# Kernel optimization log

Measured on AMD Instinct MI355X. Metric: run time of the kernel, lower is better.

## Reference

```python
import jax, jax.numpy as jnp
import numpy as np

NH = 8          # attention heads
TEMP = 2.0      # gumbel temperature


def _gumbel_softmax_hard(logits, key, temperature):
    # hard=True straight-through gumbel softmax (module is in eval mode)
    g = jax.random.gumbel(key, logits.shape, logits.dtype)
    y = jax.nn.softmax((logits + g) / temperature, axis=-1)
    y_hard = jax.nn.one_hot(jnp.argmax(y, axis=-1), logits.shape[-1], dtype=y.dtype)
    return y_hard - jax.lax.stop_gradient(y) + y


def _experts(x, w1, w2, w3):
    # SwiGLU FFN over all experts at once: x [T,C], w1/w3 [E,H,C], w2 [E,C,H] -> [T,E,C]
    h = jax.nn.silu(jnp.einsum('tc,ehc->teh', x, w1)) * jnp.einsum('tc,ehc->teh', x, w3)
    return jnp.einsum('teh,ech->tec', h, w2)


def _mha(q_in, kv_in, in_w, in_b, out_w, out_b):
    C = q_in.shape[-1]
    hd = C // NH
    q = q_in @ in_w[:C].T + in_b[:C]
    k = kv_in @ in_w[C:2 * C].T + in_b[C:2 * C]
    v = kv_in @ in_w[2 * C:].T + in_b[2 * C:]
    B, Tq, _ = q.shape
    Tk = k.shape[1]
    q = q.reshape(B, Tq, NH, hd)
    k = k.reshape(B, Tk, NH, hd)
    v = v.reshape(B, Tk, NH, hd)
    scale = jnp.asarray(1.0 / np.sqrt(hd), q.dtype)
    att = jax.nn.softmax(jnp.einsum('bqhd,bkhd->bhqk', q, k) * scale, axis=-1)
    o = jnp.einsum('bhqk,bkhd->bqhd', att, v).reshape(B, Tq, C)
    return o @ out_w.T + out_b


def setup_inputs() -> dict:
    key = jax.random.key(0)
    ks = jax.random.split(key, 20)
    B, T, S, C, E, H = 2, 2048, 77, 1024, 4, 2816
    p = lambda k, sh: jax.random.normal(k, sh, jnp.float32) * 0.02
    return {
        'x': jax.random.normal(ks[0], (B, T, C), jnp.float32),
        'time': jax.random.normal(ks[1], (B,), jnp.float32),
        'caption': jax.random.normal(ks[2], (B, S, C), jnp.float32),
        'language': jax.random.randint(ks[3], (B,), 0, 9),
        'lang_embed': p(ks[4], (9, C)),
        'lang_gate_w': p(ks[5], (E, C)),
        'lang_gate_b': jnp.zeros((E,), jnp.float32),
        'lang_w1': p(ks[6], (E, H, C)),
        'lang_w2': p(ks[7], (E, C, H)),
        'lang_w3': p(ks[8], (E, H, C)),
        'in_proj_w': p(ks[9], (3 * C, C)),
        'in_proj_b': jnp.zeros((3 * C,), jnp.float32),
        'out_proj_w': p(ks[10], (C, C)),
        'out_proj_b': jnp.zeros((C,), jnp.float32),
        'cap_gate_w': p(ks[11], (E, C)),
        'cap_gate_b': jnp.zeros((E,), jnp.float32),
        'cap_w1': p(ks[12], (E, H, C)),
        'cap_w2': p(ks[13], (E, C, H)),
        'cap_w3': p(ks[14], (E, H, C)),
    }


def reference(x, time, caption, language, lang_embed, lang_gate_w, lang_gate_b,
              lang_w1, lang_w2, lang_w3, in_proj_w, in_proj_b, out_proj_w, out_proj_b,
              cap_gate_w, cap_gate_b, cap_w1, cap_w2, cap_w3):
    B, T, C = x.shape
    x_flat = x.reshape(-1, C)                                   # [B*T, C]

    # language gating (one logit vector per batch element, repeated over T tokens)
    lang_emb = lang_embed[language]                             # [B, C]
    lang_logits = lang_emb @ lang_gate_w.T + lang_gate_b        # [B, E]
    lang_probs = _gumbel_softmax_hard(lang_logits, jax.random.key(1), TEMP)
    lang_probs = jnp.repeat(lang_probs, T, axis=0)              # [B*T, E]

    lang_outputs = _experts(x_flat, lang_w1, lang_w2, lang_w3)  # [B*T, E, C]
    first_out = (lang_outputs * lang_probs[:, :, None]).sum(axis=1)  # [B*T, C]
    first_reshaped = first_out.reshape(B, T, C)

    # cross attention against caption, then per-token caption gating
    cross = _mha(first_reshaped, caption, in_proj_w, in_proj_b, out_proj_w, out_proj_b)
    cross_flat = cross.reshape(-1, C)
    cap_logits = cross_flat @ cap_gate_w.T + cap_gate_b         # [B*T, E]
    cap_probs = _gumbel_softmax_hard(cap_logits, jax.random.key(2), TEMP)

    cap_outputs = _experts(first_out, cap_w1, cap_w2, cap_w3)   # [B*T, E, C]
    second_out = (cap_outputs * cap_probs[:, :, None]).sum(axis=1)

    total_out = (first_out + second_out).reshape(B, T, C)

    all_probs = jnp.concatenate([lang_probs, cap_probs], axis=1)  # [B*T, 2E]
    expert_usage = all_probs.mean(axis=0)
    loss = (expert_usage * jnp.log(expert_usage + 1e-10)).sum()
    return total_out, loss
```

## Files before the change

### kernel.cpp

```cpp
#include <hip/hip_runtime.h>
#include <stdint.h>

#define B_ 2
#define T_ 2048
#define S_ 77
#define C_ 1024
#define E_ 4
#define H_ 2816
#define NH_ 8
#define HD_ 128
#define N_ (B_*T_)
#define MAXGB (N_/128 + E_)
#define MAXGB2 (N_/256 + E_)
#define PEsz ((size_t)H_*C_)

typedef _Float16 h8 __attribute__((ext_vector_type(8)));
typedef _Float16 h4 __attribute__((ext_vector_type(4)));
typedef float f4 __attribute__((ext_vector_type(4)));

__device__ __forceinline__ void gload16(const void* g, void* l){
  __builtin_amdgcn_global_load_lds((const __attribute__((address_space(1))) void*)g,
                                   (__attribute__((address_space(3))) void*)l, 16, 0, 0);
}

__device__ __forceinline__ void xcd_swizzle(int& bx, int& by){
  int nx = gridDim.x, ny = gridDim.y;
  int nwg = nx*ny;
  int wg = by*nx + bx;
  int q = nwg >> 3, r = nwg & 7;
  int xcd = wg & 7, idx = wg >> 3;
  int s = (xcd < r ? xcd*(q+1) : r*(q+1) + (xcd-r)*q) + idx;
  bx = s % nx; by = s / nx;
}

__device__ __forceinline__ uint32_t rotl32(uint32_t v, int r){ return (v<<r)|(v>>(32-r)); }
__device__ __forceinline__ void threefry2x32(uint32_t k0, uint32_t k1,
                                             uint32_t x, uint32_t y,
                                             uint32_t& o0, uint32_t& o1){
  uint32_t k2 = k0 ^ k1 ^ 0x1BD11BDAu;
  x += k0; y += k1;
#define TFR(r) { x += y; y = rotl32(y, r); y ^= x; }
  TFR(13) TFR(15) TFR(26) TFR(6)   x += k1; y += k2 + 1u;
  TFR(17) TFR(29) TFR(16) TFR(24)  x += k2; y += k0 + 2u;
  TFR(13) TFR(15) TFR(26) TFR(6)   x += k0; y += k1 + 3u;
  TFR(17) TFR(29) TFR(16) TFR(24)  x += k1; y += k2 + 4u;
  TFR(13) TFR(15) TFR(26) TFR(6)   x += k2; y += k0 + 5u;
#undef TFR
  o0 = x; o1 = y;
}
__device__ __forceinline__ float gumbel_from_bits(uint32_t bits){
  const float TINY = 1.17549435e-38f;
  float f = __uint_as_float((bits >> 9) | 0x3f800000u) - 1.0f;
  float u = fmaxf(TINY, f + TINY);
  return -logf(-logf(u));
}
__device__ __forceinline__ float jax_gumbel(uint32_t k0, uint32_t k1, uint32_t idx){
  uint32_t a, b;
  threefry2x32(k0, k1, 0u, idx, a, b);
  return gumbel_from_bits(a ^ b);
}

__global__ __launch_bounds__(256) void setup_lang(
    const float* __restrict__ lang_embed, const float* __restrict__ gate_w,
    const float* __restrict__ gate_b, const int* __restrict__ language,
    float* __restrict__ langP, int* __restrict__ lang_sel, int* __restrict__ counts)
{
  __shared__ float red[256];
  __shared__ float logits[8];
  int tid = threadIdx.x;
  for (int be = 0; be < 8; ++be){
    int b = be >> 2, e = be & 3;
    const float* emb = lang_embed + (size_t)language[b] * C_;
    const float* gw  = gate_w + (size_t)e * C_;
    float p = 0.f;
    for (int c = tid; c < C_; c += 256) p += emb[c] * gw[c];
    red[tid] = p; __syncthreads();
    for (int s = 128; s > 0; s >>= 1){
      if (tid < s) red[tid] += red[tid + s];
      __syncthreads();
    }
    if (tid == 0) logits[be] = red[0] + gate_b[e];
    __syncthreads();
  }
  if (tid == 0){
    for (int b = 0; b < B_; ++b){
      float z[E_], m = -3.4e38f;
      for (int e = 0; e < E_; ++e){
        float gmb = jax_gumbel(0u, 1u, (uint32_t)(b*E_ + e));
        z[e] = (logits[b*E_ + e] + gmb) * 0.5f;
        m = fmaxf(m, z[e]);
      }
      float y[E_], sum = 0.f;
      for (int e = 0; e < E_; ++e){ y[e] = expf(z[e] - m); sum += y[e]; }
      for (int e = 0; e < E_; ++e) y[e] = y[e] / sum;
      int best = 0; float bv = y[0];
      for (int e = 1; e < E_; ++e) if (y[e] > bv){ bv = y[e]; best = e; }
      lang_sel[b] = best;
      for (int e = 0; e < E_; ++e)
        langP[b*E_ + e] = ((e == best) ? 1.0f : 0.0f) - y[e] + y[e];
    }
    for (int e = 0; e < E_; ++e) counts[e] = 0;
  }
}

__global__ __launch_bounds__(256) void conv_split(const float* __restrict__ s,
    _Float16* __restrict__ hi, _Float16* __restrict__ lo, long n4){
  long i = (long)blockIdx.x*256 + threadIdx.x;
  long stride = (long)gridDim.x*256;
  for (; i < n4; i += stride){
    float4 v = ((const float4*)s)[i];
    h4 h, L;
    h[0]=(_Float16)v.x; h[1]=(_Float16)v.y; h[2]=(_Float16)v.z; h[3]=(_Float16)v.w;
    L[0]=(_Float16)(v.x-(float)h[0]); L[1]=(_Float16)(v.y-(float)h[1]);
    L[2]=(_Float16)(v.z-(float)h[2]); L[3]=(_Float16)(v.w-(float)h[3]);
    ((h4*)hi)[i] = h; ((h4*)lo)[i] = L;
  }
}
__global__ __launch_bounds__(256) void conv_plain(const float* __restrict__ s,
    _Float16* __restrict__ d, long n4){
  long i = (long)blockIdx.x*256 + threadIdx.x;
  long stride = (long)gridDim.x*256;
  for (; i < n4; i += stride){
    float4 v = ((const float4*)s)[i];
    h4 h;
    h[0]=(_Float16)v.x; h[1]=(_Float16)v.y; h[2]=(_Float16)v.z; h[3]=(_Float16)v.w;
    ((h4*)d)[i] = h;
  }
}
__global__ __launch_bounds__(256) void conv_split_sel(const float* __restrict__ base,
    const int* __restrict__ sel, int slot,
    _Float16* __restrict__ hi, _Float16* __restrict__ lo, long n4){
  const float* s = base + (size_t)sel[slot]*PEsz;
  long i = (long)blockIdx.x*256 + threadIdx.x;
  long stride = (long)gridDim.x*256;
  for (; i < n4; i += stride){
    float4 v = ((const float4*)s)[i];
    h4 h, L;
    h[0]=(_Float16)v.x; h[1]=(_Float16)v.y; h[2]=(_Float16)v.z; h[3]=(_Float16)v.w;
    L[0]=(_Float16)(v.x-(float)h[0]); L[1]=(_Float16)(v.y-(float)h[1]);
    L[2]=(_Float16)(v.z-(float)h[2]); L[3]=(_Float16)(v.w-(float)h[3]);
    ((h4*)hi)[i] = h; ((h4*)lo)[i] = L;
  }
}
template<bool SPLIT>
__global__ __launch_bounds__(256) void conv_w13(
    const float* __restrict__ w1, const float* __restrict__ w3,
    const int* __restrict__ sel, int nslot,
    _Float16* __restrict__ hi, _Float16* __restrict__ lo)
{
  const int K8 = C_/8;
  long total = (long)nslot * (2*H_) * K8;
  for (long i = (long)blockIdx.x*256 + threadIdx.x; i < total; i += (long)gridDim.x*256){
    int kv = (int)(i & (K8-1));
    long rs = i >> 7;
    int r  = (int)(rs % (2*H_));
    int slot = (int)(rs / (2*H_));
    int e = SPLIT ? sel[slot] : slot;
    int gg = r >> 5, o = r & 31;
    const float* src = ((o<16)? w1 : w3) + (size_t)e*PEsz + (size_t)(16*gg + (o&15))*C_ + kv*8;
    float4 v0 = *(const float4*)src, v1 = *(const float4*)(src+4);
    float vv[8] = {v0.x,v0.y,v0.z,v0.w,v1.x,v1.y,v1.z,v1.w};
    h8 hh, ll;
#pragma unroll
    for (int jj=0;jj<8;++jj){
      hh[jj] = (_Float16)vv[jj];
      if constexpr (SPLIT) ll[jj] = (_Float16)(vv[jj]-(float)hh[jj]);
    }
    size_t dof = (size_t)slot*2*PEsz + (size_t)r*C_ + kv*8;
    *(h8*)(hi + dof) = hh;
    if constexpr (SPLIT) *(h8*)(lo + dof) = ll;
  }
}

__global__ __launch_bounds__(512,2) void gemm_gate_split(
    const _Float16* __restrict__ Ahi, const _Float16* __restrict__ Alo,
    const _Float16* __restrict__ Bhi, const _Float16* __restrict__ Blo,
    _Float16* __restrict__ Hhi, _Float16* __restrict__ Hlo)
{
  __shared__ __align__(16) char smem[147456];
  const int tid = threadIdx.x, w = tid>>6, l = tid&63;
  const int lm = l&15, g = l>>4;
  const int wm = w>>1, wn = w&1;
  int bx = blockIdx.x, by = blockIdx.y;
  xcd_swizzle(bx, by);
  const int n0 = bx<<7;
  const int m0 = by<<8;
  const size_t eoff = (m0 >= T_) ? (size_t)2*PEsz : 0;

  const _Float16* srcA[4]; const _Float16* srcB[2];
#pragma unroll
  for (int jj=0;jj<4;++jj){
    int c = jj*512 + tid, r = c>>3, s = c&7;
    int st = s ^ (r&7);
    srcA[jj] = (st<4 ? Ahi : Alo) + (size_t)(m0 + r)*C_ + ((st&3)<<3);
  }
#pragma unroll
  for (int jj=0;jj<2;++jj){
    int c = jj*512 + tid, r = c>>3, s = c&7;
    int st = s ^ (r&7);
    srcB[jj] = (st<4 ? Bhi : Blo) + eoff + (size_t)(n0 + r)*C_ + ((st&3)<<3);
  }

#define STG(ts, bi) { \
    int k0 = (ts)<<5; \
    char* db = smem + (bi)*49152; \
    _Pragma("unroll") \
    for (int jj=0;jj<4;++jj) gload16(srcA[jj]+k0, db + (jj*512 + w*64)*16); \
    _Pragma("unroll") \
    for (int jj=0;jj<2;++jj) gload16(srcB[jj]+k0, db + 32768 + (jj*512 + w*64)*16); \
  }

  const int shi = (g ^ (lm&7)) << 4;
  int aoff[4], boff[4];
#pragma unroll
  for (int i=0;i<4;++i){
    aoff[i] = ((wm*64 + i*16 + lm)<<7) + shi;
    boff[i] = 32768 + ((wn*64 + i*16 + lm)<<7) + shi;
  }

  f4 acc[4][4] = {};
  const int nt = C_/32;
  STG(0,0) STG(1,1)
  for (int t=0; t<nt; ++t){
    const int bi = t%3;
// ... 104 lines not shown
#pragma unroll
  for (int i=0;i<4;++i){
    aoff[i] = ((wm*64 + i*16 + lm)<<7) + shi;
    boff[i] = 32768 + ((wn*64 + i*16 + lm)<<7) + shi;
  }

  f4 acc[4][4] = {};
  const int nt = C_/64;
  STG(0,0) STG(1,1)
  for (int t=0; t<nt; ++t){
    const int bi = t%3;
    const int ts = (t+2 < nt) ? t+2 : 0;
    STG(ts, (t+2)%3)
    asm volatile("s_waitcnt vmcnt(12)" ::: "memory");
    __builtin_amdgcn_s_barrier();
    asm volatile("" ::: "memory");
    const char* base = smem + bi*49152;
#pragma unroll
    for (int kk=0;kk<2;++kk){
      h8 af[4], bf[4];
      const int x = kk<<6;
#pragma unroll
      for (int i=0;i<4;++i){ af[i] = *(const h8*)(base + (aoff[i]^x)); bf[i] = *(const h8*)(base + (boff[i]^x)); }
      __builtin_amdgcn_s_setprio(1);
#pragma unroll
      for (int mi=0;mi<4;++mi)
#pragma unroll
        for (int ni=0;ni<4;++ni)
          acc[mi][ni] = __builtin_amdgcn_mfma_f32_16x16x32_f16(af[mi], bf[ni], acc[mi][ni],0,0,0);
      __builtin_amdgcn_s_setprio(0);
    }
    asm volatile("" ::: "memory");
    __builtin_amdgcn_s_barrier();
  }
#undef STG

#pragma unroll
  for (int mi=0;mi<4;++mi){
#pragma unroll
    for (int p=0;p<2;++p){
      int hc = ((n0 + wn*64)>>1) + p*16 + lm;
#pragma unroll
      for (int j=0;j<4;++j){
        int rl = wm*64 + mi*16 + (g<<2) + j;
        if (rl >= valid) continue;
        float s1 = acc[mi][2*p][j], s3 = acc[mi][2*p+1][j];
        Hout[(size_t)(m0 + rl)*H_ + hc] = (_Float16)(s1/(1.f+expf(-s1))*s3);
      }
    }
  }
}

template<int EPI, int NSEG, int EXPM>
__global__ __launch_bounds__(256,2) void gemm8(
    const _Float16* __restrict__ A0, const _Float16* __restrict__ A1,
    const _Float16* __restrict__ B0, const _Float16* __restrict__ B1,
    const float* __restrict__ bias, float* __restrict__ Cf32,
    _Float16* __restrict__ O0, _Float16* __restrict__ O1,
    const int* __restrict__ bmap_e, const int* __restrict__ bmap_s,
    const int* __restrict__ offs, const int* __restrict__ perm,
    int M, int K, int Nw, size_t bstride_e)
{
  __shared__ __align__(16) char smem[65536];
  const int tid = threadIdx.x, w = tid>>6, l = tid&63;
  const int lm = l&15, g = l>>4;
  const int wm = w>>1, wn = w&1;
  int bx = blockIdx.x, by = blockIdx.y;
  xcd_swizzle(bx, by);
  const int n0 = bx<<7;
  int m0, valid = 128; size_t eoff = 0;
  if constexpr (EXPM==3){
    int e = bmap_e[by]; if (e<0) return;
    m0 = bmap_s[by];
    int v = offs[e+1]-m0; valid = v>128?128:v;
    eoff = (size_t)e*bstride_e;
  } else {
    m0 = by<<7;
    if constexpr (EXPM==1) eoff = (m0>=T_) ? bstride_e : 0;
  }
  const int cAe = (((tid&7) ^ ((tid>>3)&7)) << 3);
  size_t rbA[4], rbB[4];
#pragma unroll
  for (int j=0;j<4;++j){
    int r = (j<<5) + (tid>>3);
    int ia = m0 + r;
    if constexpr (EXPM==3){ ia = (ia < N_) ? ia : (N_-1); }
    else { if (ia > M-1) ia = M-1; }
    rbA[j] = (size_t)ia*K + cAe;
    rbB[j] = eoff + (size_t)(n0+r)*K + cAe;
  }
  const int tps = K>>6, nt = NSEG*tps;

#define STAGE8(tt, cc) { \
    int sg = 0; \
    if constexpr (NSEG==3){ sg = ((tt)>=2*tps) ? 2 : (((tt)>=tps)?1:0); } \
    const _Float16* Asrc = (sg==1) ? A1 : A0; \
    const _Float16* Bsrc = (sg==2) ? B1 : B0; \
    int kk0 = ((tt) - sg*tps)<<6; \
    char* db = smem + (cc)*32768 + w*1024; \
    _Pragma("unroll") \
    for (int j=0;j<4;++j) gload16(Asrc + rbA[j] + kk0, db + j*4096); \
    _Pragma("unroll") \
    for (int j=0;j<4;++j) gload16(Bsrc + rbB[j] + kk0, db + 16384 + j*4096); \
  }

  int aoff[2][4], boff[2][4];
#pragma unroll
  for (int kk=0;kk<2;++kk){
#pragma unroll
    for (int i=0;i<4;++i){
      int ra = wm*64 + i*16 + lm;
      aoff[kk][i] = (ra<<7) + (((kk<<6)+(g<<4)) ^ ((ra&7)<<4));
      int rb = wn*64 + i*16 + lm;
      boff[kk][i] = (rb<<7) + (((kk<<6)+(g<<4)) ^ ((rb&7)<<4));
    }
  }

  f4 acc[4][4] = {};
  STAGE8(0, 0)
  for (int t=0; t<nt; ++t){
    const int c = t&1;
// ... 9 lines not shown
#pragma unroll
    for (int kk=0;kk<2;++kk){
      h8 af[4], bf[4];
#pragma unroll
      for (int i=0;i<4;++i){
        af[i] = *(const h8*)(Ab + aoff[kk][i]);
        bf[i] = *(const h8*)(Bb + boff[kk][i]);
      }
      __builtin_amdgcn_s_setprio(1);
#pragma unroll
      for (int mi=0;mi<4;++mi)
#pragma unroll
        for (int ni=0;ni<4;++ni)
          acc[mi][ni] = __builtin_amdgcn_mfma_f32_16x16x32_f16(af[mi], bf[ni], acc[mi][ni],0,0,0);
      __builtin_amdgcn_s_setprio(0);
      __builtin_amdgcn_s_barrier();
    }
  }

#pragma unroll
  for (int mi=0;mi<4;++mi){
    const int rl0 = wm*64 + mi*16 + (g<<2);
#pragma unroll
    for (int ni=0;ni<4;++ni){
      int col = n0 + wn*64 + ni*16 + lm;
#pragma unroll
      for (int j=0;j<4;++j){
        int rl = rl0 + j;
        float vv = acc[mi][ni][j];
        if constexpr (EPI==0){
          int grow = m0 + rl;
          if (grow < M) Cf32[(size_t)grow*Nw + col] = vv + bias[col];
        } else if constexpr (EPI==1){
          int grow = m0 + rl;
          if (grow < M){
            float vb = vv + (bias ? bias[col] : 0.f);
            _Float16 hh = (_Float16)vb;
            O0[(size_t)grow*Nw + col] = hh;
            O1[(size_t)grow*Nw + col] = (_Float16)(vb - (float)hh);
          }
        } else {
          if (rl < valid){
            int orig = perm[m0 + rl];
            size_t o = (size_t)orig*C_ + col;
            Cf32[o] = (float)O0[o] + (float)O1[o] + vv;
          }
        }
      }
    }
  }
#undef STAGE8
}

#define SP5 5
#define KSTR 136
#define VSTR 104
__global__ __launch_bounds__(256) void attn_mfma(
    const _Float16* __restrict__ Qh, const _Float16* __restrict__ Ql,
    const _Float16* __restrict__ KVh, const _Float16* __restrict__ KVl,
    _Float16* __restrict__ AOh, _Float16* __restrict__ AOl)
{
  __shared__ __align__(16) _Float16 Usm[2*128*VSTR];
  __shared__ __align__(16) _Float16 Psm[2*64*VSTR];
  _Float16* Kh_s = Usm;
  _Float16* Kl_s = Usm + 128*VSTR;
  _Float16* VTh  = Usm;
  _Float16* VTl  = Usm + 128*VSTR;
  _Float16* Ph   = Psm;
  _Float16* Pl   = Psm + 64*VSTR;

  const int tid = threadIdx.x;
  const int w = tid>>6, l = tid&63, lm = l&15, g = l>>4;
  const int b = blockIdx.z, h = blockIdx.y, q0 = blockIdx.x<<6;
  const float scale = 0.08838834764831845f;

  for (int i = tid; i < 64*VSTR; i += 256) ((uint32_t*)Psm)[i] = 0;
  {
    int oct = tid & 15, s0 = tid >> 4;
    for (int s = s0; s < 80; s += 16){
      h8 vh = {}, vl = {};
      if (s < S_){
        size_t ga = ((size_t)(b*S_ + s))*(2*C_) + h*HD_ + oct*8;
        vh = *(const h8*)(KVh + ga);
        vl = *(const h8*)(KVl + ga);
      }
      *(h8*)(Kh_s + s*KSTR + oct*8) = vh;
      *(h8*)(Kl_s + s*KSTR + oct*8) = vl;
    }
  }
  h8 qh[4], ql[4];
  {
    size_t qrow = (size_t)(b*T_ + q0 + w*16 + lm);
    const _Float16* qph = Qh + qrow*C_ + h*HD_ + g*8;
    const _Float16* qpl = Ql + qrow*C_ + h*HD_ + g*8;
#pragma unroll
    for (int ks=0; ks<4; ++ks){ qh[ks] = *(const h8*)(qph + ks*32); ql[ks] = *(const h8*)(qpl + ks*32); }
  }
  __syncthreads();

  f4 sc[SP5] = {};
#pragma unroll
  for (int ks=0; ks<4; ++ks){
#pragma unroll
    for (int nt=0; nt<SP5; ++nt){
      h8 kh = *(const h8*)(Kh_s + (nt*16+lm)*KSTR + ks*32 + g*8);
      h8 kl = *(const h8*)(Kl_s + (nt*16+lm)*KSTR + ks*32 + g*8);
// ... 50 lines not shown
  }
  __syncthreads();

  for (int i = tid; i < 128*VSTR; i += 256) ((uint32_t*)Usm)[i] = 0;
  __syncthreads();
  {
    int oct = tid & 15, s0 = tid >> 4;
    for (int s = s0; s < S_; s += 16){
      size_t ga = ((size_t)(b*S_ + s))*(2*C_) + C_ + h*HD_ + oct*8;
      h8 vh = *(const h8*)(KVh + ga);
      h8 vl = *(const h8*)(KVl + ga);
#pragma unroll
      for (int i2=0;i2<8;++i2){
        VTh[(oct*8+i2)*VSTR + s] = vh[i2];
        VTl[(oct*8+i2)*VSTR + s] = vl[i2];
      }
    }
  }
  __syncthreads();

  h8 pah[3], pal[3];
#pragma unroll
  for (int ks=0;ks<3;++ks){
    pah[ks] = *(const h8*)(Ph + (w*16+lm)*VSTR + ks*32 + g*8);
    pal[ks] = *(const h8*)(Pl + (w*16+lm)*VSTR + ks*32 + g*8);
  }
#pragma unroll
  for (int nt=0; nt<8; ++nt){
    f4 o = {};
#pragma unroll
    for (int ks=0;ks<3;++ks){
      h8 vh = *(const h8*)(VTh + (nt*16+lm)*VSTR + ks*32 + g*8);
      h8 vl = *(const h8*)(VTl + (nt*16+lm)*VSTR + ks*32 + g*8);
      o = __builtin_amdgcn_mfma_f32_16x16x32_f16(pah[ks], vh, o,0,0,0);
      o = __builtin_amdgcn_mfma_f32_16x16x32_f16(pal[ks], vh, o,0,0,0);
      o = __builtin_amdgcn_mfma_f32_16x16x32_f16(pah[ks], vl, o,0,0,0);
    }
#pragma unroll
    for (int j=0;j<4;++j){
      size_t orow = (size_t)(b*T_ + q0 + w*16 + g*4 + j);
      size_t oa = orow*C_ + h*HD_ + nt*16 + lm;
      _Float16 hh = (_Float16)o[j];
      AOh[oa] = hh;
      AOl[oa] = (_Float16)(o[j] - (float)hh);
    }
  }
}

__global__ __launch_bounds__(256) void cap_gate(
    const float* __restrict__ CR, const float* __restrict__ gw, const float* __restrict__ gb,
    int* __restrict__ cap_sel, float* __restrict__ capP, int* __restrict__ counts)
{
  int tid = threadIdx.x, wave = tid >> 6, lane = tid & 63;
  for (int r = 0; r < 4; ++r){
    int row = (blockIdx.x << 4) + (wave << 2) + r;
    const float* xp = CR + (size_t)row * C_;
    float lg[E_];
#pragma unroll
    for (int e = 0; e < E_; ++e){
      const float* wv = gw + (size_t)e * C_;
      float p = 0.f;
      for (int c = lane; c < C_; c += 64) p += xp[c] * wv[c];
#pragma unroll
      for (int off = 32; off; off >>= 1) p += __shfl_xor(p, off);
      lg[e] = p + gb[e];
    }
    if (lane == 0){
      float z[E_], m = -3.4e38f;
      for (int e = 0; e < E_; ++e){
        float gmb = jax_gumbel(0u, 2u, (uint32_t)(row*E_ + e));
        z[e] = (lg[e] + gmb) * 0.5f;
        m = fmaxf(m, z[e]);
      }
      float y[E_], sum = 0.f;
      for (int e = 0; e < E_; ++e){ y[e] = expf(z[e] - m); sum += y[e]; }
      for (int e = 0; e < E_; ++e) y[e] = y[e] / sum;
      int best = 0; float bv = y[0];
      for (int e = 1; e < E_; ++e) if (y[e] > bv){ bv = y[e]; best = e; }
      cap_sel[row] = best;
      atomicAdd(&counts[best], 1);
      for (int e = 0; e < E_; ++e)
        capP[(size_t)row*E_ + e] = ((e == best) ? 1.0f : 0.0f) - y[e] + y[e];
    }
  }
}

__global__ void build_groups(const int* __restrict__ counts, int* __restrict__ offs,
                             int* __restrict__ cursor,
                             int* __restrict__ bmap_e, int* __restrict__ bmap_s,
                             int* __restrict__ bmap_e2, int* __restrict__ bmap_s2)
{
  offs[0] = 0;
  for (int e = 0; e < E_; ++e){ offs[e+1] = offs[e] + counts[e]; cursor[e] = offs[e]; }
  int idx = 0;
  for (int e = 0; e < E_; ++e)
    for (int s = offs[e]; s < offs[e+1]; s += 128){ bmap_e[idx] = e; bmap_s[idx] = s; ++idx; }
  for (; idx < MAXGB; ++idx) bmap_e[idx] = -1;
  int idx2 = 0;
  for (int e = 0; e < E_; ++e)
    for (int s = offs[e]; s < offs[e+1]; s += 256){ bmap_e2[idx2] = e; bmap_s2[idx2] = s; ++idx2; }
  for (; idx2 < MAXGB2; ++idx2) bmap_e2[idx2] = -1;
}

__global__ __launch_bounds__(256) void scatter_perm(
    const int* __restrict__ cap_sel, int* __restrict__ cursor, int* __restrict__ perm)
{
  int row = blockIdx.x * 256 + threadIdx.x;
  int e = cap_sel[row];
  int pos = atomicAdd(&cursor[e], 1);
  perm[pos] = row;
}

__global__ __launch_bounds__(256) void loss_kernel(
    const float* __restrict__ capP, const float* __restrict__ langP, float* __restrict__ out_loss)
{
  __shared__ float red[4][256];
  int tid = threadIdx.x;
  float p0=0.f, p1=0.f, p2=0.f, p3=0.f;
  for (int r = tid; r < N_; r += 256){
    const float* p = capP + (size_t)r*E_;
    p0 += p[0]; p1 += p[1]; p2 += p[2]; p3 += p[3];
  }
  red[0][tid]=p0; red[1][tid]=p1; red[2][tid]=p2; red[3][tid]=p3;
  __syncthreads();
  for (int s = 128; s > 0; s >>= 1){
    if (tid < s){
      red[0][tid]+=red[0][tid+s]; red[1][tid]+=red[1][tid+s];
      red[2][tid]+=red[2][tid+s]; red[3][tid]+=red[3][tid+s];
    }
    __syncthreads();
  }
  if (tid == 0){
    float loss = 0.f;
    for (int e = 0; e < E_; ++e){
      float ul = (langP[e] + langP[E_ + e]) * 0.5f;
      loss += ul * logf(ul + 1e-10f);
    }
    for (int e = 0; e < E_; ++e){
      float uc = red[e][0] * (1.0f / N_);
      loss += uc * logf(uc + 1e-10f);
    }
    out_loss[0] = loss;
  }
}

extern "C" void kernel_launch(void* const* d_in, const int* in_sizes, int n_in,
                              void* d_out, int out_size, void* d_ws, size_t ws_size,
                              hipStream_t stream)
{
  const float* x          = (const float*)d_in[0];
  const float* caption    = (const float*)d_in[2];
  const int*   language   = (const int*)  d_in[3];
  const float* lang_embed = (const float*)d_in[4];
  const float* lang_gw    = (const float*)d_in[5];
  const float* lang_gb    = (const float*)d_in[6];
  const float* lang_w1    = (const float*)d_in[7];
  const float* lang_w2    = (const float*)d_in[8];
  const float* lang_w3    = (const float*)d_in[9];
  const float* in_w       = (const float*)d_in[10];
  const float* in_b       = (const float*)d_in[11];
  const float* out_w      = (const float*)d_in[12];
  const float* out_b      = (const float*)d_in[13];
  const float* cap_gw     = (const float*)d_in[14];
  const float* cap_gb     = (const float*)d_in[15];
  const float* cap_w1     = (const float*)d_in[16];
  const float* cap_w2     = (const float*)d_in[17];
  const float* cap_w3     = (const float*)d_in[18];
  float* out = (float*)d_out;

  const size_t NC = (size_t)N_*C_;
  const size_t NHe = (size_t)N_*H_;
  const size_t KVel = (size_t)B_*S_*2*C_;
  const size_t CAPel = (size_t)B_*S_*C_;

  char* base = (char*)d_ws;
  size_t cur = 0;
  auto alloc = [&](size_t bytes)->char*{
    char* p = base + cur;
    cur += (bytes + 255) & ~(size_t)255;
    return p;
  };
  float* Qcross = (float*)alloc(NC*4);
  _Float16* Qh = (_Float16*)Qcross;
  _Float16* Ql = Qh + NC;
  char* kvreg = alloc(KVel*4);
  _Float16* KVh = (_Float16*)kvreg;
  _Float16* KVl = KVh + KVel;
  float* capP   = (float*)alloc((size_t)N_*E_*4);
  float* langP  = (float*)alloc(64);
  int* lang_sel = (int*)alloc(64);
  int* cap_sel  = (int*)alloc(N_*4);
  int* counts   = (int*)alloc(64);
  int* offs     = (int*)alloc(64);
  int* cursor   = (int*)alloc(64);
  int* bmap_e   = (int*)alloc(MAXGB*4);
  int* bmap_s   = (int*)alloc(MAXGB*4);
  int* bmap_e2  = (int*)alloc(MAXGB2*4);
  int* bmap_s2  = (int*)alloc(MAXGB2*4);
  int* perm     = (int*)alloc(N_*4);
  _Float16* xAO_hi = (_Float16*)alloc(NC*2);
  _Float16* xAO_lo = (_Float16*)alloc(NC*2);
  _Float16* cap_hi = (_Float16*)alloc(CAPel*2);
  _Float16* cap_lo = (_Float16*)alloc(CAPel*2);
  _Float16* Hb_hi  = (_Float16*)alloc(NHe*2);
  _Float16* Hb_lo  = (_Float16*)alloc(NHe*2);
  _Float16* F_hi   = (_Float16*)alloc(NC*2);
  _Float16* F_lo   = (_Float16*)alloc(NC*2);
  _Float16* Wreg = (_Float16*)alloc(2*( (size_t)3*C_*C_*2 + (size_t)C_*C_*2 + 3*4*PEsz ));
  _Float16* w13hi = Wreg;
  _Float16* w13lo = Wreg + 4*PEsz;
  _Float16* w2hi  = Wreg + 8*PEsz;
  _Float16* w2lo  = Wreg + 10*PEsz;
  _Float16* inw_hi  = Wreg;
  _Float16* inw_lo  = inw_hi + (size_t)3*C_*C_;
  _Float16* outw_hi = inw_lo + (size_t)3*C_*C_;
  _Float16* outw_lo = outw_hi + (size_t)C_*C_;
  _Float16* capw13f = outw_lo + (size_t)C_*C_;
  _Float16* capw2f  = capw13f + 8*PEsz;

  setup_lang<<<1, 256, 0, stream>>>(lang_embed, lang_gw, lang_gb, language, langP, lang_sel, counts);
  conv_w13<true><<<2048, 256, 0, stream>>>(lang_w1, lang_w3, lang_sel, 2, w13hi, w13lo);
  conv_split_sel<<<1024, 256, 0, stream>>>(lang_w2, lang_sel, 0, w2hi, w2lo, (long)(PEsz/4));
  conv_split_sel<<<1024, 256, 0, stream>>>(lang_w2, lang_sel, 1, w2hi+PEsz, w2lo+PEsz, (long)(PEsz/4));
  conv_split<<<2048, 256, 0, stream>>>(x, xAO_hi, xAO_lo, (long)(NC/4));
  conv_split<<<256, 256, 0, stream>>>(caption, cap_hi, cap_lo, (long)(CAPel/4));

  gemm_gate_split<<<dim3((2*H_)/128, N_/256), 512, 0, stream>>>(
      xAO_hi, xAO_lo, w13hi, w13lo, Hb_hi, Hb_lo);
  gemm8<1,3,1><<<dim3(C_/128, N_/128), 256, 0, stream>>>(
      Hb_hi, Hb_lo, w2hi, w2lo, nullptr, nullptr, F_hi, F_lo,
      nullptr, nullptr, nullptr, nullptr, N_, H_, C_, PEsz);

  conv_split<<<2048, 256, 0, stream>>>(in_w, inw_hi, inw_lo, (long)((size_t)3*C_*C_/4));
  conv_split<<<1024, 256, 0, stream>>>(out_w, outw_hi, outw_lo, (long)((size_t)C_*C_/4));
  conv_w13<false><<<2048, 256, 0, stream>>>(cap_w1, cap_w3, nullptr, 4, capw13f, nullptr);
  conv_plain<<<2048, 256, 0, stream>>>(cap_w2, capw2f, (long)(4*PEsz/4));

  gemm8<1,3,0><<<dim3(C_/128, N_/128), 256, 0, stream>>>(
      F_hi, F_lo, inw_hi, inw_lo, in_b, nullptr, Qh, Ql,
      nullptr, nullptr, nullptr, nullptr, N_, C_, C_, 0);
  gemm8<1,3,0><<<dim3((2*C_)/128, 2), 256, 0, stream>>>(
      cap_hi, cap_lo, inw_hi + (size_t)C_*C_, inw_lo + (size_t)C_*C_, in_b + C_,
      nullptr, KVh, KVl,
      nullptr, nullptr, nullptr, nullptr, B_*S_, C_, 2*C_, 0);
  attn_mfma<<<dim3(T_/64, NH_, B_), 256, 0, stream>>>(Qh, Ql, KVh, KVl, xAO_hi, xAO_lo);
  gemm8<0,3,0><<<dim3(C_/128, N_/128), 256, 0, stream>>>(
      xAO_hi, xAO_lo, outw_hi, outw_lo, out_b, Qcross, nullptr, nullptr,
      nullptr, nullptr, nullptr, nullptr, N_, C_, C_, 0);

  cap_gate<<<N_/16, 256, 0, stream>>>(Qcross, cap_gw, cap_gb, cap_sel, capP, counts);
  build_groups<<<1, 1, 0, stream>>>(counts, offs, cursor, bmap_e, bmap_s, bmap_e2, bmap_s2);
  scatter_perm<<<N_/256, 256, 0, stream>>>(cap_sel, cursor, perm);

  _Float16* H2 = Hb_hi;
  gemm_gate_plain<<<dim3((2*H_)/128, MAXGB2), 512, 0, stream>>>(
      F_hi, capw13f, H2, bmap_e2, bmap_s2, offs, perm);
  gemm8<2,1,3><<<dim3(C_/128, MAXGB), 256, 0, stream>>>(
      H2, nullptr, capw2f, nullptr, nullptr, out, F_hi, F_lo,
      bmap_e, bmap_s, offs, perm, N_, H_, C_, PEsz);

  loss_kernel<<<1, 256, 0, stream>>>(capP, langP, out + NC);
}
```

Baseline: 779.8 us.

## Fuse weight conversions into GEMM launches and merge small setup/finalize kernels

The language-gate setup is now computed redundantly in every block of a single conversion kernel, which also converts the selected w1/w3/w2 experts and x. The cap-weight, in_proj, out_proj and caption conversions run as extra blocks inside the FFN1 down-projection GEMM launch, and the cap_w2 conversion and KV projection share a launch with the Q projection. build_groups, scatter_perm and the loss kernel are merged into one two-block finalize kernel. cap_gate now uses more, smaller blocks. The goal is to remove launch gaps and overlap memory-bound conversions with compute-bound GEMMs. The cost is a more complex weight-buffer layout and possible contention between co-resident conversion and GEMM blocks.

```diff
diff --git a/kernel.cpp b/kernel.cpp
--- a/kernel.cpp
+++ b/kernel.cpp
@@ -13,6 +13,7 @@
 #define MAXGB (N_/128 + E_)
 #define MAXGB2 (N_/256 + E_)
 #define PEsz ((size_t)H_*C_)
+#define CC_ ((size_t)C_*C_)
 
 typedef _Float16 h8 __attribute__((ext_vector_type(8)));
 typedef _Float16 h4 __attribute__((ext_vector_type(4)));
@@ -60,54 +61,9 @@
   return gumbel_from_bits(a ^ b);
 }
 
-__global__ __launch_bounds__(256) void setup_lang(
-    const float* __restrict__ lang_embed, const float* __restrict__ gate_w,
-    const float* __restrict__ gate_b, const int* __restrict__ language,
-    float* __restrict__ langP, int* __restrict__ lang_sel, int* __restrict__ counts)
-{
-  __shared__ float red[256];
-  __shared__ float logits[8];
-  int tid = threadIdx.x;
-  for (int be = 0; be < 8; ++be){
-    int b = be >> 2, e = be & 3;
-    const float* emb = lang_embed + (size_t)language[b] * C_;
-    const float* gw  = gate_w + (size_t)e * C_;
-    float p = 0.f;
-    for (int c = tid; c < C_; c += 256) p += emb[c] * gw[c];
-    red[tid] = p; __syncthreads();
-    for (int s = 128; s > 0; s >>= 1){
-      if (tid < s) red[tid] += red[tid + s];
-      __syncthreads();
-    }
-    if (tid == 0) logits[be] = red[0] + gate_b[e];
-    __syncthreads();
-  }
-  if (tid == 0){
-    for (int b = 0; b < B_; ++b){
-      float z[E_], m = -3.4e38f;
-      for (int e = 0; e < E_; ++e){
-        float gmb = jax_gumbel(0u, 1u, (uint32_t)(b*E_ + e));
-        z[e] = (logits[b*E_ + e] + gmb) * 0.5f;
-        m = fmaxf(m, z[e]);
-      }
-      float y[E_], sum = 0.f;
-      for (int e = 0; e < E_; ++e){ y[e] = expf(z[e] - m); sum += y[e]; }
-      for (int e = 0; e < E_; ++e) y[e] = y[e] / sum;
-      int best = 0; float bv = y[0];
-      for (int e = 1; e < E_; ++e) if (y[e] > bv){ bv = y[e]; best = e; }
-      lang_sel[b] = best;
-      for (int e = 0; e < E_; ++e)
-        langP[b*E_ + e] = ((e == best) ? 1.0f : 0.0f) - y[e] + y[e];
-    }
-    for (int e = 0; e < E_; ++e) counts[e] = 0;
-  }
-}
-
-__global__ __launch_bounds__(256) void conv_split(const float* __restrict__ s,
-    _Float16* __restrict__ hi, _Float16* __restrict__ lo, long n4){
-  long i = (long)blockIdx.x*256 + threadIdx.x;
-  long stride = (long)gridDim.x*256;
-  for (; i < n4; i += stride){
+__device__ __forceinline__ void job_split(const float* __restrict__ s,
+    _Float16* __restrict__ hi, _Float16* __restrict__ lo, long n4, int b0, int nb){
+  for (long i = (long)b0*256 + threadIdx.x; i < n4; i += (long)nb*256){
     float4 v = ((const float4*)s)[i];
     h4 h, L;
     h[0]=(_Float16)v.x; h[1]=(_Float16)v.y; h[2]=(_Float16)v.z; h[3]=(_Float16)v.w;
@@ -116,46 +72,45 @@
     ((h4*)hi)[i] = h; ((h4*)lo)[i] = L;
   }
 }
-__global__ __launch_bounds__(256) void conv_plain(const float* __restrict__ s,
-    _Float16* __restrict__ d, long n4){
-  long i = (long)blockIdx.x*256 + threadIdx.x;
-  long stride = (long)gridDim.x*256;
-  for (; i < n4; i += stride){
+__device__ __forceinline__ void job_plain(const float* __restrict__ s,
+    _Float16* __restrict__ d, long n4, int b0, int nb){
+  for (long i = (long)b0*256 + threadIdx.x; i < n4; i += (long)nb*256){
     float4 v = ((const float4*)s)[i];
     h4 h;
     h[0]=(_Float16)v.x; h[1]=(_Float16)v.y; h[2]=(_Float16)v.z; h[3]=(_Float16)v.w;
     ((h4*)d)[i] = h;
   }
 }
-__global__ __launch_bounds__(256) void conv_split_sel(const float* __restrict__ base,
-    const int* __restrict__ sel, int slot,
-    _Float16* __restrict__ hi, _Float16* __restrict__ lo, long n4){
-  const float* s = base + (size_t)sel[slot]*PEsz;
-  long i = (long)blockIdx.x*256 + threadIdx.x;
-  long stride = (long)gridDim.x*256;
-  for (; i < n4; i += stride){
-    float4 v = ((const float4*)s)[i];
-    h4 h, L;
-    h[0]=(_Float16)v.x; h[1]=(_Float16)v.y; h[2]=(_Float16)v.z; h[3]=(_Float16)v.w;
-    L[0]=(_Float16)(v.x-(float)h[0]); L[1]=(_Float16)(v.y-(float)h[1]);
-    L[2]=(_Float16)(v.z-(float)h[2]); L[3]=(_Float16)(v.w-(float)h[3]);
-    ((h4*)hi)[i] = h; ((h4*)lo)[i] = L;
-  }
-}
-template<bool SPLIT>
-__global__ __launch_bounds__(256) void conv_w13(
-    const float* __restrict__ w1, const float* __restrict__ w3,
-    const int* __restrict__ sel, int nslot,
-    _Float16* __restrict__ hi, _Float16* __restrict__ lo)
-{
+__device__ __forceinline__ void job_w13_plain(const float* __restrict__ w1,
+    const float* __restrict__ w3, _Float16* __restrict__ dst, int nslot, int b0, int nb){
   const int K8 = C_/8;
   long total = (long)nslot * (2*H_) * K8;
-  for (long i = (long)blockIdx.x*256 + threadIdx.x; i < total; i += (long)gridDim.x*256){
+  for (long i = (long)b0*256 + threadIdx.x; i < total; i += (long)nb*256){
     int kv = (int)(i & (K8-1));
     long rs = i >> 7;
     int r  = (int)(rs % (2*H_));
     int slot = (int)(rs / (2*H_));
-    int e = SPLIT ? sel[slot] : slot;
+    int gg = r >> 5, o = r & 31;
+    const float* src = ((o<16)? w1 : w3) + (size_t)slot*PEsz + (size_t)(16*gg + (o&15))*C_ + kv*8;
+    float4 v0 = *(const float4*)src, v1 = *(const float4*)(src+4);
+    float vv[8] = {v0.x,v0.y,v0.z,v0.w,v1.x,v1.y,v1.z,v1.w};
+    h8 hh;
+#pragma unroll
+    for (int jj=0;jj<8;++jj) hh[jj] = (_Float16)vv[jj];
+    *(h8*)(dst + (size_t)slot*2*PEsz + (size_t)r*C_ + kv*8) = hh;
+  }
+}
+__device__ __forceinline__ void job_w13_split_sel(const float* __restrict__ w1,
+    const float* __restrict__ w3, int sel0, int sel1,
+    _Float16* __restrict__ hi, _Float16* __restrict__ lo, int b0, int nb){
+  const int K8 = C_/8;
+  long total = 2L * (2*H_) * K8;
+  for (long i = (long)b0*256 + threadIdx.x; i < total; i += (long)nb*256){
+    int kv = (int)(i & (K8-1));
+    long rs = i >> 7;
+    int r  = (int)(rs % (2*H_));
+    int slot = (int)(rs / (2*H_));
+    int e = slot ? sel1 : sel0;
     int gg = r >> 5, o = r & 31;
     const float* src = ((o<16)? w1 : w3) + (size_t)e*PEsz + (size_t)(16*gg + (o&15))*C_ + kv*8;
     float4 v0 = *(const float4*)src, v1 = *(const float4*)(src+4);
@@ -164,12 +119,82 @@
 #pragma unroll
     for (int jj=0;jj<8;++jj){
       hh[jj] = (_Float16)vv[jj];
-      if constexpr (SPLIT) ll[jj] = (_Float16)(vv[jj]-(float)hh[jj]);
+      ll[jj] = (_Float16)(vv[jj]-(float)hh[jj]);
     }
     size_t dof = (size_t)slot*2*PEsz + (size_t)r*C_ + kv*8;
     *(h8*)(hi + dof) = hh;
-    if constexpr (SPLIT) *(h8*)(lo + dof) = ll;
-  }
+    *(h8*)(lo + dof) = ll;
+  }
+}
+__device__ __forceinline__ void job_w2_split_sel(const float* __restrict__ w2,
+    int sel0, int sel1, _Float16* __restrict__ hi, _Float16* __restrict__ lo, int b0, int nb){
+  long per = (long)(PEsz/4);
+  for (long i = (long)b0*256 + threadIdx.x; i < 2*per; i += (long)nb*256){
+    int slot = (i >= per) ? 1 : 0;
+    long ii = i - (long)slot*per;
+    float4 v = ((const float4*)(w2 + (size_t)(slot?sel1:sel0)*PEsz))[ii];
+    h4 h, L;
+    h[0]=(_Float16)v.x; h[1]=(_Float16)v.y; h[2]=(_Float16)v.z; h[3]=(_Float16)v.w;
+    L[0]=(_Float16)(v.x-(float)h[0]); L[1]=(_Float16)(v.y-(float)h[1]);
+    L[2]=(_Float16)(v.z-(float)h[2]); L[3]=(_Float16)(v.w-(float)h[3]);
+    ((h4*)(hi + (size_t)slot*PEsz))[ii] = h;
+    ((h4*)(lo + (size_t)slot*PEsz))[ii] = L;
+  }
+}
+
+#define CVA_W13 1024
+#define CVA_W2  512
+#define CVA_X   256
+#define CVA_TOT (CVA_W13+CVA_W2+CVA_X)
+__global__ __launch_bounds__(256) void convA(
+    const float* __restrict__ lang_embed, const float* __restrict__ gate_w,
+    const float* __restrict__ gate_b, const int* __restrict__ language,
+    const float* __restrict__ w1, const float* __restrict__ w3, const float* __restrict__ w2,
+    const float* __restrict__ x,
+    _Float16* __restrict__ w13hi, _Float16* __restrict__ w13lo,
+    _Float16* __restrict__ w2hi, _Float16* __restrict__ w2lo,
+    _Float16* __restrict__ xhi, _Float16* __restrict__ xlo,
+    float* __restrict__ langP, int* __restrict__ counts)
+{
+  __shared__ float lds8[8];
+  const int tid = threadIdx.x, w = tid>>6, l = tid&63;
+  for (int p = 2*w; p < 2*w+2; ++p){
+    int b = p>>2, e = p&3;
+    const float* emb = lang_embed + (size_t)language[b]*C_;
+    const float* gw  = gate_w + (size_t)e*C_;
+    float acc = 0.f;
+    for (int c = l; c < C_; c += 64) acc += emb[c]*gw[c];
+#pragma unroll
+    for (int off = 32; off; off >>= 1) acc += __shfl_xor(acc, off);
+    if (l == 0) lds8[p] = acc + gate_b[e];
+  }
+  __syncthreads();
+  int sel[2];
+  for (int b = 0; b < 2; ++b){
+    float z[4], m = -3.4e38f;
+    for (int e = 0; e < 4; ++e){
+      float g = jax_gumbel(0u, 1u, (uint32_t)(b*4 + e));
+      z[e] = (lds8[b*4 + e] + g) * 0.5f;
+      m = fmaxf(m, z[e]);
+    }
+    float y[4], sum = 0.f;
+    for (int e = 0; e < 4; ++e){ y[e] = expf(z[e]-m); sum += y[e]; }
+    for (int e = 0; e < 4; ++e) y[e] = y[e] / sum;
+    int best = 0; float bv = y[0];
+    for (int e = 1; e < 4; ++e) if (y[e] > bv){ bv = y[e]; best = e; }
+    sel[b] = best;
+    if (blockIdx.x == 0 && tid == 0){
+      for (int e = 0; e < 4; ++e)
+        langP[b*4 + e] = ((e == best) ? 1.0f : 0.0f) - y[e] + y[e];
+    }
+  }
+  if (blockIdx.x == 0 && tid == 0){
+    for (int e = 0; e < 4; ++e) counts[e] = 0;
+  }
+  int bid = blockIdx.x;
+  if (bid < CVA_W13)                 job_w13_split_sel(w1, w3, sel[0], sel[1], w13hi, w13lo, bid, CVA_W13);
+  else if (bid < CVA_W13+CVA_W2)     job_w2_split_sel(w2, sel[0], sel[1], w2hi, w2lo, bid-CVA_W13, CVA_W2);
+  else                               job_split(x, xhi, xlo, (long)((size_t)N_*C_/4), bid-CVA_W13-CVA_W2, CVA_X);
 }
 
 __global__ __launch_bounds__(512,2) void gemm_gate_split(
@@ -380,21 +405,19 @@
 }
 
 template<int EPI, int NSEG, int EXPM>
-__global__ __launch_bounds__(256,2) void gemm8(
+__device__ __forceinline__ void gemm8_body(
+    char* smem,
     const _Float16* __restrict__ A0, const _Float16* __restrict__ A1,
     const _Float16* __restrict__ B0, const _Float16* __restrict__ B1,
     const float* __restrict__ bias, float* __restrict__ Cf32,
     _Float16* __restrict__ O0, _Float16* __restrict__ O1,
     const int* __restrict__ bmap_e, const int* __restrict__ bmap_s,
     const int* __restrict__ offs, const int* __restrict__ perm,
-    int M, int K, int Nw, size_t bstride_e)
-{
-  __shared__ __align__(16) char smem[65536];
+    int M, int K, int Nw, size_t bstride_e, int bx, int by)
+{
   const int tid = threadIdx.x, w = tid>>6, l = tid&63;
   const int lm = l&15, g = l>>4;
   const int wm = w>>1, wn = w&1;
-  int bx = blockIdx.x, by = blockIdx.y;
-  xcd_swizzle(bx, by);
   const int n0 = bx<<7;
   int m0, valid = 128; size_t eoff = 0;
   if constexpr (EXPM==3){
@@ -510,6 +533,75 @@
 #undef STAGE8
 }
 
+template<int EPI, int NSEG, int EXPM>
+__global__ __launch_bounds__(256,2) void gemm8(
+    const _Float16* __restrict__ A0, const _Float16* __restrict__ A1,
+    const _Float16* __restrict__ B0, const _Float16* __restrict__ B1,
+    const float* __restrict__ bias, float* __restrict__ Cf32,
+    _Float16* __restrict__ O0, _Float16* __restrict__ O1,
+    const int* __restrict__ bmap_e, const int* __restrict__ bmap_s,
+    const int* __restrict__ offs, const int* __restrict__ perm,
+    int M, int K, int Nw, size_t bstride_e)
+{
+  __shared__ __align__(16) char smem[65536];
+  int bx = blockIdx.x, by = blockIdx.y;
+  xcd_swizzle(bx, by);
+  gemm8_body<EPI,NSEG,EXPM>(smem, A0,A1,B0,B1,bias,Cf32,O0,O1,
+                            bmap_e,bmap_s,offs,perm,M,K,Nw,bstride_e,bx,by);
+}
+
+__global__ __launch_bounds__(256,2) void ffn1_out_fused(
+    const _Float16* __restrict__ Hbh, const _Float16* __restrict__ Hbl,
+    const _Float16* __restrict__ w2hi, const _Float16* __restrict__ w2lo,
+    _Float16* __restrict__ Fh, _Float16* __restrict__ Fl,
+    const float* __restrict__ in_w, const float* __restrict__ out_w,
+    const float* __restrict__ cap_w1, const float* __restrict__ cap_w3,
+    const float* __restrict__ caption,
+    _Float16* __restrict__ inwh, _Float16* __restrict__ inwl,
+    _Float16* __restrict__ outwh, _Float16* __restrict__ outwl,
+    _Float16* __restrict__ capw13,
+    _Float16* __restrict__ caph, _Float16* __restrict__ capl)
+{
+  __shared__ __align__(16) char smem[65536];
+  int id = blockIdx.x;
+  if (id < 256){
+    int s = (id&7)*32 + (id>>3);
+    gemm8_body<1,3,1>(smem, Hbh, Hbl, w2hi, w2lo, nullptr, nullptr, Fh, Fl,
+                      nullptr,nullptr,nullptr,nullptr, N_, H_, C_, PEsz, s&7, s>>3);
+  } else {
+    int cid = id - 256;
+    if (cid < 320)      job_w13_plain(cap_w1, cap_w3, capw13, 4, cid, 320);
+    else if (cid < 448) job_split(in_w, inwh, inwl, (long)(3*CC_/4), cid-320, 128);
+    else if (cid < 496) job_split(out_w, outwh, outwl, (long)(CC_/4), cid-448, 48);
+    else                job_split(caption, caph, capl, (long)((size_t)B_*S_*C_/4), cid-496, 16);
+  }
+}
+
+__global__ __launch_bounds__(256,2) void gemm_qkv(
+    const _Float16* __restrict__ Fh, const _Float16* __restrict__ Fl,
+    const _Float16* __restrict__ caph, const _Float16* __restrict__ capl,
+    const _Float16* __restrict__ inwh, const _Float16* __restrict__ inwl,
+    const float* __restrict__ in_b,
+    _Float16* __restrict__ Qh, _Float16* __restrict__ Ql,
+    _Float16* __restrict__ KVh, _Float16* __restrict__ KVl,
+    const float* __restrict__ cap_w2, _Float16* __restrict__ capw2f)
+{
+  __shared__ __align__(16) char smem[65536];
+  int id = blockIdx.x;
+  if (id < 256){
+    int s = (id&7)*32 + (id>>3);
+    gemm8_body<1,3,0>(smem, Fh, Fl, inwh, inwl, in_b, nullptr, Qh, Ql,
+                      nullptr,nullptr,nullptr,nullptr, N_, C_, C_, 0, s&7, s>>3);
+  } else if (id < 288){
+    int cid = id - 256;
+    gemm8_body<1,3,0>(smem, caph, capl, inwh + CC_, inwl + CC_, in_b + C_,
+                      nullptr, KVh, KVl, nullptr,nullptr,nullptr,nullptr,
+                      B_*S_, C_, 2*C_, 0, cid & 15, cid >> 4);
+  } else {
+    job_plain(cap_w2, capw2f, (long)(4*PEsz/4), id-288, 96);
+  }
+}
+
 #define SP5 5
 #define KSTR 136
 #define VSTR 104
@@ -666,8 +758,8 @@
     int* __restrict__ cap_sel, float* __restrict__ capP, int* __restrict__ counts)
 {
   int tid = threadIdx.x, wave = tid >> 6, lane = tid & 63;
-  for (int r = 0; r < 4; ++r){
-    int row = (blockIdx.x << 4) + (wave << 2) + r;
+  for (int r = 0; r < 2; ++r){
+    int row = (blockIdx.x << 3) + (wave << 1) + r;
     const float* xp = CR + (size_t)row * C_;
     float lg[E_];
 #pragma unroll
@@ -699,62 +791,66 @@
   }
 }
 
-__global__ void build_groups(const int* __restrict__ counts, int* __restrict__ offs,
-                             int* __restrict__ cursor,
-                             int* __restrict__ bmap_e, int* __restrict__ bmap_s,
-                             int* __restrict__ bmap_e2, int* __restrict__ bmap_s2)
-{
-  offs[0] = 0;
-  for (int e = 0; e < E_; ++e){ offs[e+1] = offs[e] + counts[e]; cursor[e] = offs[e]; }
-  int idx = 0;
-  for (int e = 0; e < E_; ++e)
-    for (int s = offs[e]; s < offs[e+1]; s += 128){ bmap_e[idx] = e; bmap_s[idx] = s; ++idx; }
-  for (; idx < MAXGB; ++idx) bmap_e[idx] = -1;
-  int idx2 = 0;
-  for (int e = 0; e < E_; ++e)
-    for (int s = offs[e]; s < offs[e+1]; s += 256){ bmap_e2[idx2] = e; bmap_s2[idx2] = s; ++idx2; }
-  for (; idx2 < MAXGB2; ++idx2) bmap_e2[idx2] = -1;
-}
-
-__global__ __launch_bounds__(256) void scatter_perm(
-    const int* __restrict__ cap_sel, int* __restrict__ cursor, int* __restrict__ perm)
-{
-  int row = blockIdx.x * 256 + threadIdx.x;
-  int e = cap_sel[row];
-  int pos = atomicAdd(&cursor[e], 1);
-  perm[pos] = row;
-}
-
-__global__ __launch_bounds__(256) void loss_kernel(
-    const float* __restrict__ capP, const float* __restrict__ langP, float* __restrict__ out_loss)
-{
+__global__ __launch_bounds__(256) void finalize(
+    const int* __restrict__ counts, const int* __restrict__ cap_sel,
+    int* __restrict__ offs,
+    int* __restrict__ bmap_e, int* __restrict__ bmap_s,
+    int* __restrict__ bmap_e2, int* __restrict__ bmap_s2,
+    int* __restrict__ perm,
+    const float* __restrict__ capP, const float* __restrict__ langP,
+    float* __restrict__ out_loss)
+{
+  __shared__ int loffs[5];
+  __shared__ int lcur[4];
   __shared__ float red[4][256];
   int tid = threadIdx.x;
-  float p0=0.f, p1=0.f, p2=0.f, p3=0.f;
-  for (int r = tid; r < N_; r += 256){
-    const float* p = capP + (size_t)r*E_;
-    p0 += p[0]; p1 += p[1]; p2 += p[2]; p3 += p[3];
-  }
-  red[0][tid]=p0; red[1][tid]=p1; red[2][tid]=p2; red[3][tid]=p3;
-  __syncthreads();
-  for (int s = 128; s > 0; s >>= 1){
-    if (tid < s){
-      red[0][tid]+=red[0][tid+s]; red[1][tid]+=red[1][tid+s];
-      red[2][tid]+=red[2][tid+s]; red[3][tid]+=red[3][tid+s];
+  if (blockIdx.x == 0){
+    if (tid == 0){
+      loffs[0] = 0;
+      for (int e = 0; e < E_; ++e){ loffs[e+1] = loffs[e] + counts[e]; lcur[e] = loffs[e]; }
+      for (int e = 0; e < E_+1; ++e) offs[e] = loffs[e];
+      int idx = 0;
+      for (int e = 0; e < E_; ++e)
+        for (int s = loffs[e]; s < loffs[e+1]; s += 128){ bmap_e[idx] = e; bmap_s[idx] = s; ++idx; }
+      for (; idx < MAXGB; ++idx) bmap_e[idx] = -1;
+      int idx2 = 0;
+      for (int e = 0; e < E_; ++e)
+        for (int s = loffs[e]; s < loffs[e+1]; s += 256){ bmap_e2[idx2] = e; bmap_s2[idx2] = s; ++idx2; }
+      for (; idx2 < MAXGB2; ++idx2) bmap_e2[idx2] = -1;
     }
     __syncthreads();
-  }
-  if (tid == 0){
-    float loss = 0.f;
-    for (int e = 0; e < E_; ++e){
-      float ul = (langP[e] + langP[E_ + e]) * 0.5f;
-      loss += ul * logf(ul + 1e-10f);
-    }
-    for (int e = 0; e < E_; ++e){
-      float uc = red[e][0] * (1.0f / N_);
-      loss += uc * logf(uc + 1e-10f);
-    }
-    out_loss[0] = loss;
+    for (int row = tid; row < N_; row += 256){
+      int e = cap_sel[row];
+      int pos = atomicAdd(&lcur[e], 1);
+      perm[pos] = row;
+    }
+  } else {
+    float p0=0.f, p1=0.f, p2=0.f, p3=0.f;
+    for (int r = tid; r < N_; r += 256){
+      const float* p = capP + (size_t)r*E_;
+      p0 += p[0]; p1 += p[1]; p2 += p[2]; p3 += p[3];
+    }
+    red[0][tid]=p0; red[1][tid]=p1; red[2][tid]=p2; red[3][tid]=p3;
+    __syncthreads();
+    for (int s = 128; s > 0; s >>= 1){
+      if (tid < s){
+        red[0][tid]+=red[0][tid+s]; red[1][tid]+=red[1][tid+s];
+        red[2][tid]+=red[2][tid+s]; red[3][tid]+=red[3][tid+s];
+      }
+      __syncthreads();
+    }
+    if (tid == 0){
+      float loss = 0.f;
+      for (int e = 0; e < E_; ++e){
+        float ul = (langP[e] + langP[E_ + e]) * 0.5f;
+        loss += ul * logf(ul + 1e-10f);
+      }
+      for (int e = 0; e < E_; ++e){
+        float uc = red[e][0] * (1.0f / N_);
+        loss += uc * logf(uc + 1e-10f);
+      }
+      out_loss[0] = loss;
+    }
   }
 }
 
@@ -820,58 +916,52 @@
   _Float16* Hb_lo  = (_Float16*)alloc(NHe*2);
   _Float16* F_hi   = (_Float16*)alloc(NC*2);
   _Float16* F_lo   = (_Float16*)alloc(NC*2);
-  _Float16* Wreg = (_Float16*)alloc(2*( (size_t)3*C_*C_*2 + (size_t)C_*C_*2 + 3*4*PEsz ));
+  _Float16* Wreg = (_Float16*)alloc(2*( (size_t)3*CC_*2 + CC_*2 + 3*4*PEsz ));
   _Float16* w13hi = Wreg;
   _Float16* w13lo = Wreg + 4*PEsz;
   _Float16* w2hi  = Wreg + 8*PEsz;
   _Float16* w2lo  = Wreg + 10*PEsz;
-  _Float16* inw_hi  = Wreg;
-  _Float16* inw_lo  = inw_hi + (size_t)3*C_*C_;
-  _Float16* outw_hi = inw_lo + (size_t)3*C_*C_;
-  _Float16* outw_lo = outw_hi + (size_t)C_*C_;
-  _Float16* capw13f = outw_lo + (size_t)C_*C_;
-  _Float16* capw2f  = capw13f + 8*PEsz;
-
-  setup_lang<<<1, 256, 0, stream>>>(lang_embed, lang_gw, lang_gb, language, langP, lang_sel, counts);
-  conv_w13<true><<<2048, 256, 0, stream>>>(lang_w1, lang_w3, lang_sel, 2, w13hi, w13lo);
-  conv_split_sel<<<1024, 256, 0, stream>>>(lang_w2, lang_sel, 0, w2hi, w2lo, (long)(PEsz/4));
-  conv_split_sel<<<1024, 256, 0, stream>>>(lang_w2, lang_sel, 1, w2hi+PEsz, w2lo+PEsz, (long)(PEsz/4));
-  conv_split<<<2048, 256, 0, stream>>>(x, xAO_hi, xAO_lo, (long)(NC/4));
-  conv_split<<<256, 256, 0, stream>>>(caption, cap_hi, cap_lo, (long)(CAPel/4));
+  _Float16* capw13f = Wreg;
+  _Float16* capw2f  = Wreg + 8*PEsz;
+  _Float16* inw_hi  = Wreg + 12*PEsz;
+  _Float16* inw_lo  = inw_hi + 3*CC_;
+  _Float16* outw_hi = inw_lo + 3*CC_;
+  _Float16* outw_lo = outw_hi + CC_;
+  (void)lang_sel; (void)cursor;
+
+  convA<<<CVA_TOT, 256, 0, stream>>>(
+      lang_embed, lang_gw, lang_gb, language,
+      lang_w1, lang_w3, lang_w2, x,
+      w13hi, w13lo, w2hi, w2lo, xAO_hi, xAO_lo, langP, counts);
 
   gemm_gate_split<<<dim3((2*H_)/128, N_/256), 512, 0, stream>>>(
       xAO_hi, xAO_lo, w13hi, w13lo, Hb_hi, Hb_lo);
-  gemm8<1,3,1><<<dim3(C_/128, N_/128), 256, 0, stream>>>(
-      Hb_hi, Hb_lo, w2hi, w2lo, nullptr, nullptr, F_hi, F_lo,
-      nullptr, nullptr, nullptr, nullptr, N_, H_, C_, PEsz);
-
-  conv_split<<<2048, 256, 0, stream>>>(in_w, inw_hi, inw_lo, (long)((size_t)3*C_*C_/4));
-  conv_split<<<1024, 256, 0, stream>>>(out_w, outw_hi, outw_lo, (long)((size_t)C_*C_/4));
-  conv_w13<false><<<2048, 256, 0, stream>>>(cap_w1, cap_w3, nullptr, 4, capw13f, nullptr);
-  conv_plain<<<2048, 256, 0, stream>>>(cap_w2, capw2f, (long)(4*PEsz/4));
-
-  gemm8<1,3,0><<<dim3(C_/128, N_/128), 256, 0, stream>>>(
-      F_hi, F_lo, inw_hi, inw_lo, in_b, nullptr, Qh, Ql,
-      nullptr, nullptr, nullptr, nullptr, N_, C_, C_, 0);
-  gemm8<1,3,0><<<dim3((2*C_)/128, 2), 256, 0, stream>>>(
-      cap_hi, cap_lo, inw_hi + (size_t)C_*C_, inw_lo + (size_t)C_*C_, in_b + C_,
-      nullptr, KVh, KVl,
-      nullptr, nullptr, nullptr, nullptr, B_*S_, C_, 2*C_, 0);
+
+  ffn1_out_fused<<<768, 256, 0, stream>>>(
+      Hb_hi, Hb_lo, w2hi, w2lo, F_hi, F_lo,
+      in_w, out_w, cap_w1, cap_w3, caption,
+      inw_hi, inw_lo, outw_hi, outw_lo, capw13f, cap_hi, cap_lo);
+
+  gemm_qkv<<<384, 256, 0, stream>>>(
+      F_hi, F_lo, cap_hi, cap_lo, inw_hi, inw_lo, in_b,
+      Qh, Ql, KVh, KVl, cap_w2, capw2f);
+
   attn_mfma<<<dim3(T_/64, NH_, B_), 256, 0, stream>>>(Qh, Ql, KVh, KVl, xAO_hi, xAO_lo);
+
   gemm8<0,3,0><<<dim3(C_/128, N_/128), 256, 0, stream>>>(
       xAO_hi, xAO_lo, outw_hi, outw_lo, out_b, Qcross, nullptr, nullptr,
       nullptr, nullptr, nullptr, nullptr, N_, C_, C_, 0);
 
-  cap_gate<<<N_/16, 256, 0, stream>>>(Qcross, cap_gw, cap_gb, cap_sel, capP, counts);
-  build_groups<<<1, 1, 0, stream>>>(counts, offs, cursor, bmap_e, bmap_s, bmap_e2, bmap_s2);
-  scatter_perm<<<N_/256, 256, 0, stream>>>(cap_sel, cursor, perm);
+  cap_gate<<<N_/8, 256, 0, stream>>>(Qcross, cap_gw, cap_gb, cap_sel, capP, counts);
+
+  finalize<<<2, 256, 0, stream>>>(counts, cap_sel, offs, bmap_e, bmap_s,
+                                  bmap_e2, bmap_s2, perm, capP, langP, out + NC);
 
   _Float16* H2 = Hb_hi;
   gemm_gate_plain<<<dim3((2*H_)/128, MAXGB2), 512, 0, stream>>>(
       F_hi, capw13f, H2, bmap_e2, bmap_s2, offs, perm);
+
   gemm8<2,1,3><<<dim3(C_/128, MAXGB), 256, 0, stream>>>(
       H2, nullptr, capw2f, nullptr, nullptr, out, F_hi, F_lo,
       bmap_e, bmap_s, offs, perm, N_, H_, C_, PEsz);
-
-  loss_kernel<<<1, 256, 0, stream>>>(capP, langP, out + NC);
-}
+}
```

Result: faster. 690.6 us (-11.4%).
